# Performance work log

Hardware: AMD Instinct MI355X
Metric: run time of the kernel (lower is better)

Reference implementation:

```python
import jax, jax.numpy as jnp
import numpy as np

ALPHA = 0.2          # LeakyReLU negative slope
NEG_FILL = -9e15     # mask value used by the original module


def setup_inputs() -> dict:
    key = jax.random.key(0)
    k1, k2, k3, k4 = jax.random.split(key, 4)
    N, D, H, F = 4096, 512, 8, 64  # nhid*nheads == embedding_dim
    h = jax.random.normal(k1, (N, D), dtype=jnp.float32)
    adj = jax.random.randint(k2, (N, N), 0, 2, dtype=jnp.int32)
    # per-head linear projection weights (no bias) and attention vectors
    W = jax.random.normal(k3, (H, D, F), dtype=jnp.float32) * (1.0 / np.sqrt(D))
    a = jax.random.normal(k4, (H, 2 * F), dtype=jnp.float32) * 0.1
    return {"h": h, "adj": adj, "W": W, "a": a}


def reference(h, adj, W, a):
    H, D, F = W.shape
    N = h.shape[0]
    # per-head projection: [H, N, F]
    hp = jnp.einsum('nd,hdf->hnf', h, W)
    # score(i,j) = leakyrelu(a[:F].h_i + a[F:].h_j)  (decomposed broadcast-add,
    # same math as the original N*N concat construction)
    a_src, a_dst = a[:, :F], a[:, F:]
    f_src = jnp.einsum('hnf,hf->hn', hp, a_src)  # [H, N]
    f_dst = jnp.einsum('hnf,hf->hn', hp, a_dst)  # [H, N]
    e = jax.nn.leaky_relu(f_src[:, :, None] + f_dst[:, None, :], ALPHA)  # [H,N,N]
    e = jnp.where(adj[None] > 0, e, NEG_FILL)
    att = jax.nn.softmax(e, axis=-1)  # softmax over neighbors j (dim=1 in torch)
    out = jnp.einsum('hij,hjf->hif', att, hp)  # [H, N, F]
    # concat heads -> [N, H*F], then ELU
    out = jnp.transpose(out, (1, 0, 2)).reshape(N, H * F)
    return jax.nn.elu(out)
```

## Files before the change

### kernel.cpp

```cpp
#include <hip/hip_runtime.h>

#define NN 4096
#define DD 512
#define HH 8
#define FF 64
#define LRELU_ALPHA 0.2f
#define SP 72

typedef __attribute__((ext_vector_type(8))) short bf16x8;
typedef __attribute__((ext_vector_type(4))) float f32x4;

__device__ __forceinline__ float f4c(const float4& v, int k) {
    return k == 0 ? v.x : (k == 1 ? v.y : (k == 2 ? v.z : v.w));
}
__device__ __forceinline__ void f4s(float4& v, int k, float x) {
    if (k == 0) v.x = x; else if (k == 1) v.y = x; else if (k == 2) v.z = x; else v.w = x;
}
__device__ __forceinline__ unsigned short f2bf(float x) {
    unsigned u = __float_as_uint(x);
    return (unsigned short)((u + 0x7fffu + ((u >> 16) & 1u)) >> 16);
}
__device__ __forceinline__ float bf2f(unsigned short h) {
    return __uint_as_float(((unsigned)h) << 16);
}
__device__ __forceinline__ unsigned fkey(float x) {
    unsigned u = __float_as_uint(x);
    return (u & 0x80000000u) ? ~u : (u | 0x80000000u);
}
__device__ __forceinline__ float funkey(unsigned k) {
    unsigned u = (k & 0x80000000u) ? (k ^ 0x80000000u) : ~k;
    return __uint_as_float(u);
}

__global__ __launch_bounds__(256) void k_prep(const int* __restrict__ adj,
                                              const float* __restrict__ W,
                                              unsigned* __restrict__ adjw,
                                              unsigned short* __restrict__ wt_hi,
                                              unsigned short* __restrict__ wt_lo,
                                              unsigned* __restrict__ mxkey,
                                              float* __restrict__ hpsum) {
    __shared__ float tile[64][65];
    int b = blockIdx.x, t = threadIdx.x;
    if (b < 4096) {
        int lane = t & 63;
        #pragma unroll
        for (int i = 0; i < 16; i++) {
            int tid = ((b * 16 + i) << 8) + t;
            unsigned long long mask = __ballot(adj[tid] > 0);
            if (lane == 0) {
                int base = tid >> 5;
                adjw[base] = (unsigned)mask;
                adjw[base + 1] = (unsigned)(mask >> 32);
            }
        }
    } else if (b < 4160) {
        int idx = b - 4096;
        int h = idx >> 3;
        int d0 = (idx & 7) * 64;
        #pragma unroll
        for (int kidx = 0; kidx < 4; kidx++) {
            int id = t + 256 * kidx;
            int dd = id >> 4, f4i = (id & 15) * 4;
            float4 v = *(const float4*)(W + ((size_t)(h * DD + d0 + dd)) * FF + f4i);
            tile[dd][f4i] = v.x; tile[dd][f4i + 1] = v.y;
            tile[dd][f4i + 2] = v.z; tile[dd][f4i + 3] = v.w;
        }
        __syncthreads();
        int f = t >> 2, c = (t & 3) * 16;
        union { unsigned short s[16]; uint4 v[2]; } hb, lb;
        #pragma unroll
        for (int q = 0; q < 16; q++) {
            float v = tile[c + q][f];
            unsigned short hi = f2bf(v);
            hb.s[q] = hi;
            lb.s[q] = f2bf(v - bf2f(hi));
        }
        uint4* dh = (uint4*)(wt_hi + ((size_t)h * FF + f) * DD + d0 + c);
        uint4* dl = (uint4*)(wt_lo + ((size_t)h * FF + f) * DD + d0 + c);
        dh[0] = hb.v[0]; dh[1] = hb.v[1];
        dl[0] = lb.v[0]; dl[1] = lb.v[1];
    } else {
        if (t < 16) mxkey[t] = 0u;
        hpsum[t] = 0.f;
        hpsum[t + 256] = 0.f;
    }
}

__global__ __launch_bounds__(256) void k_hp_mfma(const float* __restrict__ hmat,
                                                 const unsigned short* __restrict__ whi,
                                                 const unsigned short* __restrict__ wlo,
                                                 const float* __restrict__ a,
                                                 unsigned short* __restrict__ hpT_hi,
                                                 float* __restrict__ fs,
                                                 float* __restrict__ fd,
                                                 float* __restrict__ hpsum,
                                                 unsigned* __restrict__ mxkey) {
    __shared__ char smem[4 * 64 * SP * 2];
    unsigned short* ah = (unsigned short*)smem;
    unsigned short* al = ah + 64 * SP;
    unsigned short* bh = al + 64 * SP;
    unsigned short* bl = bh + 64 * SP;

    int t = threadIdx.x;
    int h = blockIdx.y;
    int n0 = blockIdx.x * 64;
    int lane = t & 63;
    int w = t >> 6;
    int R0 = (w >> 1) * 32, F0 = (w & 1) * 32;
    int am = lane & 15, aq = lane >> 4;
    int sr = t >> 2, sc = (t & 3) * 16;

    const float* gha = hmat + (size_t)(n0 + sr) * DD;
    const unsigned short* gbh = whi + ((size_t)h * FF + sr) * DD;
    const unsigned short* gbl = wlo + ((size_t)h * FF + sr) * DD;

    f32x4 acc[2][2] = {};
    for (int kk = 0; kk < DD; kk += 64) {
        {
            float4 p0 = *(const float4*)(gha + kk + sc);
            float4 p1 = *(const float4*)(gha + kk + sc + 4);
            float4 p2 = *(const float4*)(gha + kk + sc + 8);
            float4 p3 = *(const float4*)(gha + kk + sc + 12);
            union { unsigned short s[16]; uint4 v[2]; } hb, lb;
            #pragma unroll
            for (int q = 0; q < 16; q++) {
                float v = q < 4 ? f4c(p0, q) : q < 8 ? f4c(p1, q - 4)
                          : q < 12 ? f4c(p2, q - 8) : f4c(p3, q - 12);
                unsigned short hi = f2bf(v);
                hb.s[q] = hi;
                lb.s[q] = f2bf(v - bf2f(hi));
            }
            *(uint4*)(ah + sr * SP + sc) = hb.v[0]; *(uint4*)(ah + sr * SP + sc + 8) = hb.v[1];
            *(uint4*)(al + sr * SP + sc) = lb.v[0]; *(uint4*)(al + sr * SP + sc + 8) = lb.v[1];
        }
        {
            const uint4* s2 = (const uint4*)(gbh + kk + sc);
            const uint4* s3 = (const uint4*)(gbl + kk + sc);
            uint4 w0 = s2[0], w1 = s2[1], x0 = s3[0], x1 = s3[1];
            *(uint4*)(bh + sr * SP + sc) = w0; *(uint4*)(bh + sr * SP + sc + 8) = w1;
            *(uint4*)(bl + sr * SP + sc) = x0; *(uint4*)(bl + sr * SP + sc + 8) = x1;
        }
        __syncthreads();
        #pragma unroll
        for (int k2 = 0; k2 < 2; k2++) {
            int ko = k2 * 32 + aq * 8;
            bf16x8 a0h = *(const bf16x8*)(ah + (R0 + am) * SP + ko);
            bf16x8 a1h = *(const bf16x8*)(ah + (R0 + 16 + am) * SP + ko);
            bf16x8 a0l = *(const bf16x8*)(al + (R0 + am) * SP + ko);
            bf16x8 a1l = *(const bf16x8*)(al + (R0 + 16 + am) * SP + ko);
            bf16x8 b0h = *(const bf16x8*)(bh + (F0 + am) * SP + ko);
            bf16x8 b1h = *(const bf16x8*)(bh + (F0 + 16 + am) * SP + ko);
            bf16x8 b0l = *(const bf16x8*)(bl + (F0 + am) * SP + ko);
            bf16x8 b1l = *(const bf16x8*)(bl + (F0 + 16 + am) * SP + ko);
            acc[0][0] = __builtin_amdgcn_mfma_f32_16x16x32_bf16(a0h, b0h, acc[0][0], 0, 0, 0);
            acc[0][1] = __builtin_amdgcn_mfma_f32_16x16x32_bf16(a0h, b1h, acc[0][1], 0, 0, 0);
            acc[1][0] = __builtin_amdgcn_mfma_f32_16x16x32_bf16(a1h, b0h, acc[1][0], 0, 0, 0);
            acc[1][1] = __builtin_amdgcn_mfma_f32_16x16x32_bf16(a1h, b1h, acc[1][1], 0, 0, 0);
            acc[0][0] = __builtin_amdgcn_mfma_f32_16x16x32_bf16(a0h, b0l, acc[0][0], 0, 0, 0);
            acc[0][1] = __builtin_amdgcn_mfma_f32_16x16x32_bf16(a0h, b1l, acc[0][1], 0, 0, 0);
            acc[1][0] = __builtin_amdgcn_mfma_f32_16x16x32_bf16(a1h, b0l, acc[1][0], 0, 0, 0);
            acc[1][1] = __builtin_amdgcn_mfma_f32_16x16x32_bf16(a1h, b1l, acc[1][1], 0, 0, 0);
            acc[0][0] = __builtin_amdgcn_mfma_f32_16x16x32_bf16(a0l, b0h, acc[0][0], 0, 0, 0);
            acc[0][1] = __builtin_amdgcn_mfma_f32_16x16x32_bf16(a0l, b1h, acc[0][1], 0, 0, 0);
            acc[1][0] = __builtin_amdgcn_mfma_f32_16x16x32_bf16(a1l, b0h, acc[1][0], 0, 0, 0);
            acc[1][1] = __builtin_amdgcn_mfma_f32_16x16x32_bf16(a1l, b1h, acc[1][1], 0, 0, 0);
        }
        __syncthreads();
    }

    unsigned* tt = (unsigned*)smem;
    float* rs = (float*)(smem + 17408);
    float* rd = rs + 256;
    float* ash = rd + 256;
    if (t < 128) ash[t] = a[h * 2 * FF + t];
    int col = lane & 15, rbase = (lane >> 4) * 4;
    #pragma unroll
    for (int m16 = 0; m16 < 2; m16++) {
        #pragma unroll
        for (int n16 = 0; n16 < 2; n16++) {
            #pragma unroll
            for (int r = 0; r < 4; r++) {
                int nl = R0 + m16 * 16 + rbase + r;
                int f = F0 + n16 * 16 + col;
                float v = acc[m16][n16][r];
                unsigned short hi = f2bf(v);
                unsigned short lo = f2bf(v - bf2f(hi));
                tt[f * 68 + nl] = (unsigned)hi | ((unsigned)lo << 16);
            }
        }
    }
    __syncthreads();
    {
        int f = t >> 2, c = (t & 3) * 16;
        union { unsigned short s[16]; uint4 v[2]; } hb;
        float csum = 0.f;
        #pragma unroll
        for (int q = 0; q < 16; q++) {
            unsigned u = tt[f * 68 + c + q];
            hb.s[q] = (unsigned short)(u & 0xffffu);
            csum += bf2f((unsigned short)(u & 0xffffu)) + bf2f((unsigned short)(u >> 16));
        }
        uint4* dh = (uint4*)(hpT_hi + ((size_t)h * FF + f) * NN + n0 + c);
        dh[0] = hb.v[0]; dh[1] = hb.v[1];
        csum += __shfl_xor(csum, 1);
        csum += __shfl_xor(csum, 2);
        if ((t & 3) == 0) unsafeAtomicAdd(hpsum + h * FF + f, csum);
    }
    {
        int n = t & 63, g = t >> 6;
        float fsp = 0.f, fdp = 0.f;
        #pragma unroll
        for (int q = 0; q < 16; q++) {
            int f = g * 16 + q;
            unsigned u = tt[f * 68 + n];
            float v = bf2f((unsigned short)(u & 0xffffu)) + bf2f((unsigned short)(u >> 16));
            fsp += v * ash[f];
            fdp += v * ash[64 + f];
        }
        rs[g * 64 + n] = fsp;
        rd[g * 64 + n] = fdp;
    }
    __syncthreads();
    if (t < 64) {
        float fdv = rd[t] + rd[64 + t] + rd[128 + t] + rd[192 + t];
        fs[(size_t)h * NN + n0 + t] = rs[t] + rs[64 + t] + rs[128 + t] + rs[192 + t];
        fd[(size_t)h * NN + n0 + t] = fdv;
        unsigned key = fkey(fdv);
        #pragma unroll
        for (int off = 32; off; off >>= 1) key = max(key, (unsigned)__shfl_xor((int)key, off));
        if (t == 0) atomicMax(mxkey + h, key);
    }
}

__global__ __launch_bounds__(256) void k_attn(const float* __restrict__ fs,
                                              const float* __restrict__ fd,
                                              const unsigned* __restrict__ mxkey,
                                              const unsigned* __restrict__ adjw,
                                              const unsigned short* __restrict__ hpT_hi,
                                              const float* __restrict__ hpsum,
                                              float* __restrict__ outp) {
    __shared__ unsigned short pa[2][32 * SP];
    __shared__ unsigned short hbh[2][64 * SP];
    __shared__ float fss[32], ms[32];

    int t = threadIdx.x;
    int h = blockIdx.y;
    int i0 = blockIdx.x * 32;
    int lane = t & 63;
    int w = t >> 6;

    const float LOG2E = 1.44269504f;
    float mfd = funkey(mxkey[h]);
    if (t < 32) {
        float fsv = fs[(size_t)h * NN + i0 + t];
        fss[t] = fsv;
        float s = fsv + mfd;
        float m = fmaxf(s, LRELU_ALPHA * s);
        ms[t] = m * LOG2E;
    }
    __syncthreads();

    int wr = t >> 3;
    int wc = (t & 7) * 8;
    int sr = t >> 2, sc = (t & 3) * 16;
    int R0 = (w >> 1) * 16, F0 = (w & 1) * 32;
    int am = lane & 15, aq = lane >> 4;
    f32x4 acc[2] = {};
    f32x4 accl = {};
    bf16x8 bones;
    #pragma unroll
    for (int i = 0; i < 8; i++) bones[i] = (short)0x3f80;

    const unsigned short* gH = hpT_hi + (size_t)h * FF * NN;
    const float* fdh = fd + (size_t)h * NN;
    float fsr = fss[wr], mr = ms[wr];

    auto produce = [&](int j0, int buf) {
        {
            const uint4* sh = (const uint4*)(gH + (size_t)sr * NN + j0 + sc);
            uint4 v0 = sh[0], v1 = sh[1];
            *(uint4*)(&hbh[buf][sr * SP + sc]) = v0;
            *(uint4*)(&hbh[buf][sr * SP + sc + 8]) = v1;
        }
        {
            unsigned word = adjw[(size_t)(i0 + wr) * (NN / 32) + ((j0 + wc) >> 5)];
            unsigned bits = word >> (wc & 31);
            union { unsigned u[4]; uint4 v; } wb;
            #pragma unroll
            for (int q = 0; q < 2; q++) {
                float4 fdv = *(const float4*)(fdh + j0 + wc + q * 4);
                unsigned eu[4];
                #pragma unroll
                for (int b = 0; b < 4; b++) {
                    float s = fsr + f4c(fdv, b);
                    float l = fmaxf(s, LRELU_ALPHA * s);
                    float e = __builtin_amdgcn_exp2f(__builtin_fmaf(l, LOG2E, -mr));
                    e = ((bits >> (q * 4 + b)) & 1u) ? e : 0.f;
                    eu[b] = __float_as_uint(e);
                }
                wb.u[q * 2]     = __builtin_amdgcn_perm(eu[1], eu[0], 0x07060302);
                wb.u[q * 2 + 1] = __builtin_amdgcn_perm(eu[3], eu[2], 0x07060302);
            }
            *(uint4*)(&pa[buf][wr * SP + wc]) = wb.v;
        }
    };

    produce(0, 0);
    __syncthreads();
    for (int j0 = 0; j0 < NN; j0 += 64) {
        int cur = (j0 >> 6) & 1;
        if (j0 + 64 < NN) produce(j0 + 64, cur ^ 1);
        #pragma unroll
        for (int k2 = 0; k2 < 2; k2++) {
            int ko = k2 * 32 + aq * 8;
            bf16x8 a0 = *(const bf16x8*)(&pa[cur][(R0 + am) * SP + ko]);
            bf16x8 b0 = *(const bf16x8*)(&hbh[cur][(F0 + am) * SP + ko]);
            bf16x8 b1 = *(const bf16x8*)(&hbh[cur][(F0 + 16 + am) * SP + ko]);
            acc[0] = __builtin_amdgcn_mfma_f32_16x16x32_bf16(a0, b0, acc[0], 0, 0, 0);
            acc[1] = __builtin_amdgcn_mfma_f32_16x16x32_bf16(a0, b1, acc[1], 0, 0, 0);
            accl   = __builtin_amdgcn_mfma_f32_16x16x32_bf16(a0, bones, accl, 0, 0, 0);
        }
        __syncthreads();
    }

    const float invN = 1.0f / NN;
    int col = lane & 15, rbase = (lane >> 4) * 4;
    #pragma unroll
    for (int r = 0; r < 4; r++) {
        int row = i0 + R0 + rbase + r;
        float l = accl[r];
        float rl = 1.f / l;
        #pragma unroll
        for (int n16 = 0; n16 < 2; n16++) {
            int f = F0 + n16 * 16 + col;
            float v;
            if (l > 0.f) v = acc[n16][r] * rl;
            else         v = hpsum[h * FF + f] * invN;
            v = v > 0.f ? v : __expf(v) - 1.f;
            outp[(size_t)row * (HH * FF) + h * FF + f] = v;
        }
    }
}

extern "C" void kernel_launch(void* const* d_in, const int* in_sizes, int n_in,
                              void* d_out, int out_size, void* d_ws, size_t ws_size,
                              hipStream_t stream) {
    const float* hmat = (const float*)d_in[0];
    const int*   adj  = (const int*)d_in[1];
    const float* W    = (const float*)d_in[2];
    const float* a    = (const float*)d_in[3];
    float* out = (float*)d_out;

    char* ws = (char*)d_ws;
    unsigned short* hpT_hi = (unsigned short*)(ws);
    unsigned*       adjw   = (unsigned*)(ws + (4u << 20));
    unsigned short* wt_hi  = (unsigned short*)(ws + (6u << 20));
    unsigned short* wt_lo  = (unsigned short*)(ws + (6u << 20) + (512u << 10));
    float* fs    = (float*)(ws + (7u << 20));
    float* fd    = (float*)(ws + (7u << 20) + (128u << 10));
    unsigned* mxkey = (unsigned*)(ws + (7u << 20) + (256u << 10));
    float* hpsum = (float*)(mxkey + 16);

    k_prep   <<<dim3(4161),          256, 0, stream>>>(adj, W, adjw, wt_hi, wt_lo,
                                                       mxkey, hpsum);
    k_hp_mfma<<<dim3(64, 8),         256, 0, stream>>>(hmat, wt_hi, wt_lo, a,
                                                       hpT_hi, fs, fd, hpsum, mxkey);
    k_attn   <<<dim3(NN / 32, HH),   256, 0, stream>>>(fs, fd, mxkey, adjw,
                                                       hpT_hi, hpsum, out);
}
```

Measured before the change: 189.5 us.

## Prefetch next tiles into registers and use barriers that skip the vmcnt wait

Both the projection GEMM loop and the attention aggregation loop now split tile staging into a global-to-register load and a register-to-LDS write. The next tile's global loads are issued before the barrier so their latency overlaps the MFMA work on the current tile. __syncthreads is replaced by an inline-asm barrier that waits only on lgkmcnt, so outstanding global loads are not drained at each barrier. This holds more live registers, which risks lower occupancy, and relies on the asm barrier being correct for LDS ordering.

```diff
diff --git a/kernel.cpp b/kernel.cpp
--- a/kernel.cpp
+++ b/kernel.cpp
@@ -30,6 +30,9 @@
 __device__ __forceinline__ float funkey(unsigned k) {
     unsigned u = (k & 0x80000000u) ? (k ^ 0x80000000u) : ~k;
     return __uint_as_float(u);
+}
+__device__ __forceinline__ void sync_lds() {
+    asm volatile("s_waitcnt lgkmcnt(0)\n\ts_barrier" ::: "memory");
 }
 
 __global__ __launch_bounds__(256) void k_prep(const int* __restrict__ adj,
@@ -114,33 +117,39 @@
     const unsigned short* gbh = whi + ((size_t)h * FF + sr) * DD;
     const unsigned short* gbl = wlo + ((size_t)h * FF + sr) * DD;
 
+    float4 p0, p1, p2, p3;
+    uint4 w0, w1, x0, x1;
+    auto gload = [&](int kk) {
+        p0 = *(const float4*)(gha + kk + sc);
+        p1 = *(const float4*)(gha + kk + sc + 4);
+        p2 = *(const float4*)(gha + kk + sc + 8);
+        p3 = *(const float4*)(gha + kk + sc + 12);
+        const uint4* s2 = (const uint4*)(gbh + kk + sc);
+        const uint4* s3 = (const uint4*)(gbl + kk + sc);
+        w0 = s2[0]; w1 = s2[1]; x0 = s3[0]; x1 = s3[1];
+    };
+    auto wstage = [&]() {
+        union { unsigned short s[16]; uint4 v[2]; } hb, lb;
+        #pragma unroll
+        for (int q = 0; q < 16; q++) {
+            float v = q < 4 ? f4c(p0, q) : q < 8 ? f4c(p1, q - 4)
+                      : q < 12 ? f4c(p2, q - 8) : f4c(p3, q - 12);
+            unsigned short hi = f2bf(v);
+            hb.s[q] = hi;
+            lb.s[q] = f2bf(v - bf2f(hi));
+        }
+        *(uint4*)(ah + sr * SP + sc) = hb.v[0]; *(uint4*)(ah + sr * SP + sc + 8) = hb.v[1];
+        *(uint4*)(al + sr * SP + sc) = lb.v[0]; *(uint4*)(al + sr * SP + sc + 8) = lb.v[1];
+        *(uint4*)(bh + sr * SP + sc) = w0; *(uint4*)(bh + sr * SP + sc + 8) = w1;
+        *(uint4*)(bl + sr * SP + sc) = x0; *(uint4*)(bl + sr * SP + sc + 8) = x1;
+    };
+
     f32x4 acc[2][2] = {};
+    gload(0);
     for (int kk = 0; kk < DD; kk += 64) {
-        {
-            float4 p0 = *(const float4*)(gha + kk + sc);
-            float4 p1 = *(const float4*)(gha + kk + sc + 4);
-            float4 p2 = *(const float4*)(gha + kk + sc + 8);
-            float4 p3 = *(const float4*)(gha + kk + sc + 12);
-            union { unsigned short s[16]; uint4 v[2]; } hb, lb;
-            #pragma unroll
-            for (int q = 0; q < 16; q++) {
-                float v = q < 4 ? f4c(p0, q) : q < 8 ? f4c(p1, q - 4)
-                          : q < 12 ? f4c(p2, q - 8) : f4c(p3, q - 12);
-                unsigned short hi = f2bf(v);
-                hb.s[q] = hi;
-                lb.s[q] = f2bf(v - bf2f(hi));
-            }
-            *(uint4*)(ah + sr * SP + sc) = hb.v[0]; *(uint4*)(ah + sr * SP + sc + 8) = hb.v[1];
-            *(uint4*)(al + sr * SP + sc) = lb.v[0]; *(uint4*)(al + sr * SP + sc + 8) = lb.v[1];
-        }
-        {
-            const uint4* s2 = (const uint4*)(gbh + kk + sc);
-            const uint4* s3 = (const uint4*)(gbl + kk + sc);
-            uint4 w0 = s2[0], w1 = s2[1], x0 = s3[0], x1 = s3[1];
-            *(uint4*)(bh + sr * SP + sc) = w0; *(uint4*)(bh + sr * SP + sc + 8) = w1;
-            *(uint4*)(bl + sr * SP + sc) = x0; *(uint4*)(bl + sr * SP + sc + 8) = x1;
-        }
-        __syncthreads();
+        wstage();
+        if (kk + 64 < DD) gload(kk + 64);
+        sync_lds();
         #pragma unroll
         for (int k2 = 0; k2 < 2; k2++) {
             int ko = k2 * 32 + aq * 8;
@@ -165,7 +174,7 @@
             acc[1][0] = __builtin_amdgcn_mfma_f32_16x16x32_bf16(a1l, b0h, acc[1][0], 0, 0, 0);
             acc[1][1] = __builtin_amdgcn_mfma_f32_16x16x32_bf16(a1l, b1h, acc[1][1], 0, 0, 0);
         }
-        __syncthreads();
+        sync_lds();
     }
 
     unsigned* tt = (unsigned*)smem;
@@ -275,41 +284,45 @@
     const float* fdh = fd + (size_t)h * NN;
     float fsr = fss[wr], mr = ms[wr];
 
-    auto produce = [&](int j0, int buf) {
-        {
-            const uint4* sh = (const uint4*)(gH + (size_t)sr * NN + j0 + sc);
-            uint4 v0 = sh[0], v1 = sh[1];
-            *(uint4*)(&hbh[buf][sr * SP + sc]) = v0;
-            *(uint4*)(&hbh[buf][sr * SP + sc + 8]) = v1;
-        }
-        {
-            unsigned word = adjw[(size_t)(i0 + wr) * (NN / 32) + ((j0 + wc) >> 5)];
-            unsigned bits = word >> (wc & 31);
-            union { unsigned u[4]; uint4 v; } wb;
+    uint4 rH0, rH1;
+    float4 rF0, rF1;
+    unsigned rA;
+    auto gload = [&](int j0) {
+        const uint4* sh = (const uint4*)(gH + (size_t)sr * NN + j0 + sc);
+        rH0 = sh[0]; rH1 = sh[1];
+        rF0 = *(const float4*)(fdh + j0 + wc);
+        rF1 = *(const float4*)(fdh + j0 + wc + 4);
+        rA  = adjw[(size_t)(i0 + wr) * (NN / 32) + ((j0 + wc) >> 5)];
+    };
+    auto wstage = [&](int buf) {
+        *(uint4*)(&hbh[buf][sr * SP + sc]) = rH0;
+        *(uint4*)(&hbh[buf][sr * SP + sc + 8]) = rH1;
+        unsigned bits = rA >> (wc & 31);
+        union { unsigned u[4]; uint4 v; } wb;
+        #pragma unroll
+        for (int q = 0; q < 2; q++) {
+            float4 fdv = q ? rF1 : rF0;
+            unsigned eu[4];
             #pragma unroll
-            for (int q = 0; q < 2; q++) {
-                float4 fdv = *(const float4*)(fdh + j0 + wc + q * 4);
-                unsigned eu[4];
-                #pragma unroll
-                for (int b = 0; b < 4; b++) {
-                    float s = fsr + f4c(fdv, b);
-                    float l = fmaxf(s, LRELU_ALPHA * s);
-                    float e = __builtin_amdgcn_exp2f(__builtin_fmaf(l, LOG2E, -mr));
-                    e = ((bits >> (q * 4 + b)) & 1u) ? e : 0.f;
-                    eu[b] = __float_as_uint(e);
-                }
-                wb.u[q * 2]     = __builtin_amdgcn_perm(eu[1], eu[0], 0x07060302);
-                wb.u[q * 2 + 1] = __builtin_amdgcn_perm(eu[3], eu[2], 0x07060302);
+            for (int b = 0; b < 4; b++) {
+                float s = fsr + f4c(fdv, b);
+                float l = fmaxf(s, LRELU_ALPHA * s);
+                float e = __builtin_amdgcn_exp2f(__builtin_fmaf(l, LOG2E, -mr));
+                e = ((bits >> (q * 4 + b)) & 1u) ? e : 0.f;
+                eu[b] = __float_as_uint(e);
             }
-            *(uint4*)(&pa[buf][wr * SP + wc]) = wb.v;
-        }
+            wb.u[q * 2]     = __builtin_amdgcn_perm(eu[1], eu[0], 0x07060302);
+            wb.u[q * 2 + 1] = __builtin_amdgcn_perm(eu[3], eu[2], 0x07060302);
+        }
+        *(uint4*)(&pa[buf][wr * SP + wc]) = wb.v;
     };
 
-    produce(0, 0);
-    __syncthreads();
-    for (int j0 = 0; j0 < NN; j0 += 64) {
-        int cur = (j0 >> 6) & 1;
-        if (j0 + 64 < NN) produce(j0 + 64, cur ^ 1);
+    gload(0);
+    wstage(0);
+    gload(64);
+    sync_lds();
+    for (int k = 0; k < NN / 64; k++) {
+        int cur = k & 1;
         #pragma unroll
         for (int k2 = 0; k2 < 2; k2++) {
             int ko = k2 * 32 + aq * 8;
@@ -320,7 +333,11 @@
             acc[1] = __builtin_amdgcn_mfma_f32_16x16x32_bf16(a0, b1, acc[1], 0, 0, 0);
             accl   = __builtin_amdgcn_mfma_f32_16x16x32_bf16(a0, bones, accl, 0, 0, 0);
         }
-        __syncthreads();
+        if (k < NN / 64 - 1) {
+            wstage(cur ^ 1);
+            if (k < NN / 64 - 2) gload((k + 2) * 64);
+        }
+        sync_lds();
     }
 
     const float invN = 1.0f / NN;
```

New measurement: 190.0 us. No clear change (+0.3%).
